# Optimization experiments

Measured on AMD Instinct MI355X. Metric: run time of the kernel, lower is better.

## Reference

```python
import jax, jax.numpy as jnp
import numpy as np

N = 65536   # query points
M = 65536   # support points
H = 32      # neighbors per query
IN = 64     # input feature dim
OUT = 64    # out_dim // 2
K = 15      # kernel points
EXTENT = 0.1 * 1.2 / 2.5  # radius * kp_extent / conv_radius = 0.048
BN_EPS = 1e-5


def setup_inputs() -> dict:
    key = jax.random.key(0)
    ks = jax.random.split(key, 8)
    x = jax.random.normal(ks[0], (M, IN), dtype=jnp.float32)
    q_pts = jax.random.uniform(ks[1], (N, 3), dtype=jnp.float32) * 0.1
    s_pts = jax.random.uniform(ks[2], (M, 3), dtype=jnp.float32) * 0.1
    neighb_inds = jax.random.randint(ks[3], (N, H), 0, M, dtype=jnp.int32)
    kernel_points = jax.random.normal(ks[4], (K, 3), dtype=jnp.float32) * (0.5 * EXTENT)
    weights = jax.random.normal(ks[5], (K, IN, OUT), dtype=jnp.float32) * 0.05
    gamma = jnp.ones((OUT,), dtype=jnp.float32)
    beta = jnp.zeros((OUT,), dtype=jnp.float32)
    return {"x": x, "q_pts": q_pts, "s_pts": s_pts, "neighb_inds": neighb_inds,
            "kernel_points": kernel_points, "weights": weights,
            "gamma": gamma, "beta": beta}


def reference(x, q_pts, s_pts, neighb_inds, kernel_points, weights, gamma, beta):
    # --- KPConv (rigid, linear influence, sum aggregation) ---
    # Shadow point/feature for out-of-range neighbor indices (KPConv convention).
    s_pad = jnp.concatenate([s_pts, jnp.full((1, 3), 1e6, s_pts.dtype)], axis=0)
    x_pad = jnp.concatenate([x, jnp.zeros((1, x.shape[1]), x.dtype)], axis=0)

    # Relative neighbor coordinates: [N, H, 3]
    neighbors = s_pad[neighb_inds] - q_pts[:, None, :]
    # Squared distance to each kernel point: [N, H, K]
    diffs = neighbors[:, :, None, :] - kernel_points[None, None, :, :]
    sq_dist = jnp.sum(diffs * diffs, axis=-1)
    # Linear kernel-point influence, clipped at 0: [N, H, K]
    all_weights = jnp.maximum(1.0 - jnp.sqrt(sq_dist) / EXTENT, 0.0)

    # Gather neighbor features: [N, H, IN]
    neighb_x = x_pad[neighb_inds]
    # Influence-weighted aggregation per kernel point: [N, K, IN]
    weighted = jnp.einsum('nhk,nhi->nki', all_weights, neighb_x)
    # Apply per-kernel-point weight matrices and sum over kernel points: [N, OUT]
    out = jnp.einsum('nki,kio->no', weighted, weights)

    # --- BatchNorm (training-mode statistics over points) ---
    mean = jnp.mean(out, axis=0)
    var = jnp.var(out, axis=0)
    out = (out - mean) / jnp.sqrt(var + BN_EPS) * gamma + beta

    # --- LeakyReLU(0.1) ---
    return jnp.where(out >= 0, out, 0.1 * out)
```

## Files before the change

kernel.cpp:

```cpp
#include <hip/hip_runtime.h>
#include <math.h>

#define NQ   65536
#define H    32
#define IN   64
#define OUTC 64
#define K    15
#define QB   16
#define INV_EXT (1.0f / 0.048f)

#define OFF_PSUM  131072
#define OFF_SCSH  (OFF_PSUM + 2097152)
#define OFF_XBF   (OFF_SCSH + 1024)
#define NEED_BF16 (OFF_XBF + (size_t)NQ * IN * 2)

typedef __attribute__((ext_vector_type(8))) short short8;
typedef __attribute__((ext_vector_type(4))) short short4v;
typedef __attribute__((ext_vector_type(4))) float float4v;

static __device__ __forceinline__ unsigned short f2bf(float f) {
    return (unsigned short)((__float_as_uint(f) + 0x8000u) >> 16);
}
static __device__ __forceinline__ unsigned pk2(float a, float b) {
    return (__float_as_uint(a) + 0x8000u) >> 16 |
           ((__float_as_uint(b) + 0x8000u) & 0xFFFF0000u);
}

__global__ __launch_bounds__(256) void prep_all(
    const float* __restrict__ W, const float* __restrict__ x,
    short* __restrict__ Bfrag, unsigned short* __restrict__ xbf, int do_x)
{
    const int b = blockIdx.x;
    if (b < 4096) {
        if (do_x) {
            const int t = b * 256 + threadIdx.x;
            const float4 v = ((const float4*)x)[t];
            uint2 p; p.x = pk2(v.x, v.y); p.y = pk2(v.z, v.w);
            ((uint2*)xbf)[t] = p;
        }
    } else {
        const int t2  = (b - 4096) * 256 + threadIdx.x;
        const int j   = t2 & 7;
        const int ln  = (t2 >> 3) & 63;
        const int tt  = (t2 >> 9) & 31;
        const int wvq = t2 >> 14;
        const int kp2 = tt * 32 + (ln >> 4) * 8 + j;
        const int kq  = kp2 & 15;
        const int ii  = kp2 >> 4;
        const int oo  = wvq * 16 + (ln & 15);
        const float val = (kq < K) ? W[(kq * 64 + ii) * 64 + oo] : 0.0f;
        Bfrag[t2] = (short)f2bf(val);
    }
}

template<bool BFX>
__global__ __launch_bounds__(256, 5) void kpconv_mfma(
    const float* __restrict__ x, const unsigned short* __restrict__ xbf,
    const float* __restrict__ qp, const float* __restrict__ sp,
    const int* __restrict__ inds, const float* __restrict__ kp,
    const short* __restrict__ Bfrag, float* __restrict__ out_raw,
    float* __restrict__ psum)
{
    __shared__ __align__(16) short lds[16384];
    short* xn  = lds;
    short* wT2 = lds + 8192;

    const int tid  = threadIdx.x;
    const int lane = tid & 63;
    const int wv   = tid >> 6;
    const int quad = lane >> 4;
    const int ml   = lane & 15;
    const int q0   = blockIdx.x * QB;

    const int q8x = (((lane >> 3) & 1) << 2) | (lane & 3);
    const int m8x = (((lane >> 4) & 3) << 1) | ((lane >> 2) & 1);
    const int hbase = ((q8x >> 2) << 4) | (q8x & 3);

    short* xn_own = xn + wv * 2048;

    short8 xv[4][4];
    float4 xf[4][4][2];
#pragma unroll
    for (int qi = 0; qi < 4; ++qi) {
        const int ibase = (q0 + wv * 4 + qi) * H;
#pragma unroll
        for (int j = 0; j < 4; ++j) {
            const int id = inds[ibase + hbase + j * 4];
            if (BFX) {
                xv[qi][j] = *(const short8*)((const short*)xbf + id * IN + m8x * 8);
            } else {
                xf[qi][j][0] = *(const float4*)(x + id * IN + m8x * 8);
                xf[qi][j][1] = *(const float4*)(x + id * IN + m8x * 8 + 4);
            }
        }
    }

#pragma unroll
    for (int rep = 0; rep < 2; ++rep) {
        const int p  = lane + rep * 64;
        const int qi = p >> 5, h = p & 31;
        const int qg = wv * 4 + qi;
        const int n  = q0 + qg;
        const int id = inds[n * H + h];
        const float dx = sp[id * 3 + 0] - qp[n * 3 + 0];
        const float dy = sp[id * 3 + 1] - qp[n * 3 + 1];
        const float dz = sp[id * 3 + 2] - qp[n * 3 + 2];
        short8 w0, w1;
#pragma unroll
        for (int k = 0; k < K; ++k) {
            const float ex = dx - kp[k * 3 + 0];
            const float ey = dy - kp[k * 3 + 1];
            const float ez = dz - kp[k * 3 + 2];
            const float sq = ex * ex + ey * ey + ez * ez;
            float wval = 1.0f - __builtin_amdgcn_sqrtf(sq) * INV_EXT;
            wval = wval > 0.0f ? wval : 0.0f;
            if (k < 8) w0[k]     = (short)f2bf(wval);
            else       w1[k - 8] = (short)f2bf(wval);
        }
        w1[7] = 0;
        short* dst = wT2 + qg * 512 + ((h >> 2) & 1) * 256 + (h >> 3) * 64 + (h & 3) * 16;
        *(short8*)dst       = w0;
        *(short8*)(dst + 8) = w1;
    }

    const unsigned ldsb = (unsigned)(size_t)(&lds[0]);
    const unsigned xnb  = ldsb + (unsigned)(wv * 4096 + lane * 8);
    const unsigned wtb  = ldsb + 16384u + (unsigned)(wv * 4096 + lane * 8);

    float4v frag[4][4];
#pragma unroll
    for (int qi = 0; qi < 4; ++qi)
#pragma unroll
        for (int v = 0; v < 4; ++v) frag[qi][v] = (float4v){0.f, 0.f, 0.f, 0.f};

    const int EbBase = (m8x >> 1) * 512 + (q8x >> 2) * 128 + (q8x & 3) * 16 + (m8x & 1) * 8;

#pragma unroll
    for (int qi = 0; qi < 4; ++qi) {
#pragma unroll
        for (int j = 0; j < 4; ++j) {
            short8 pv;
            if (BFX) {
                pv = xv[qi][j];
            } else {
                const float4 a0 = xf[qi][j][0], a1 = xf[qi][j][1];
                pv[0] = (short)f2bf(a0.x); pv[1] = (short)f2bf(a0.y);
                pv[2] = (short)f2bf(a0.z); pv[3] = (short)f2bf(a0.w);
                pv[4] = (short)f2bf(a1.x); pv[5] = (short)f2bf(a1.y);
                pv[6] = (short)f2bf(a1.z); pv[7] = (short)f2bf(a1.w);
            }
            *(short8*)&xn_own[EbBase + (j & 1) * 256 + (j >> 1) * 64] = pv;
        }
        __builtin_amdgcn_sched_barrier(0);

        short4v a0, a1, b0[4], b1[4];
        asm volatile("ds_read_b64_tr_b16 %0, %1 offset:%c2"
                     : "=v"(a0) : "v"(wtb), "i"(qi * 1024) : "memory");
        asm volatile("ds_read_b64_tr_b16 %0, %1 offset:%c2"
                     : "=v"(a1) : "v"(wtb), "i"(qi * 1024 + 512) : "memory");
#pragma unroll
        for (int v = 0; v < 4; ++v) {
            asm volatile("ds_read_b64_tr_b16 %0, %1 offset:%c2"
                         : "=v"(b0[v]) : "v"(xnb), "i"(v * 1024) : "memory");
            asm volatile("ds_read_b64_tr_b16 %0, %1 offset:%c2"
                         : "=v"(b1[v]) : "v"(xnb), "i"(v * 1024 + 512) : "memory");
        }
        asm volatile("s_waitcnt lgkmcnt(0)");
        __builtin_amdgcn_sched_barrier(0);

        short8 a;
#pragma unroll
        for (int e = 0; e < 4; ++e) { a[e] = a0[e]; a[e + 4] = a1[e]; }
#pragma unroll
        for (int v = 0; v < 4; ++v) {
            short8 bb;
#pragma unroll
            for (int e = 0; e < 4; ++e) { bb[e] = b0[v][e]; bb[e + 4] = b1[v][e]; }
            frag[qi][v] = __builtin_amdgcn_mfma_f32_16x16x32_bf16(a, bb, frag[qi][v], 0, 0, 0);
        }
    }

    __syncthreads();

    char* AwtB = (char*)lds;
#pragma unroll
    for (int qi = 0; qi < 4; ++qi) {
        const int qg = wv * 4 + qi;
        char* qb = AwtB + qg * 2048;
        const int xr = ((qg & 7) << 4) ^ (((qg >> 3) & 1) << 3) ^ ((ml >> 2) << 3);
#pragma unroll
        for (int v = 0; v < 4; ++v) {
            short4v w;
#pragma unroll
            for (int r = 0; r < 4; ++r) w[r] = (short)f2bf(frag[qi][v][r]);
            const int Bw = (v * 16 + ml) * 32 + quad * 8;
            *(short4v*)(qb + (Bw ^ xr)) = w;
        }
    }
    __syncthreads();

    float4v acc = (float4v){0.f, 0.f, 0.f, 0.f};
    const short* bptr = Bfrag + (wv * 32) * 512 + lane * 8;
    const char*  arow = AwtB + ml * 2048;
    const int    xr2  = ((ml & 7) << 4) ^ (((ml >> 3) & 1) << 3);
#pragma unroll 2
    for (int t = 0; t < 32; ++t) {
        const int Br = t * 64 + quad * 16;
        const int ad = (Br ^ xr2 ^ (((t >> 1) & 3) << 3));
        const short4v alo = *(const short4v*)(arow + ad);
        const short4v ahi = *(const short4v*)(arow + (ad ^ 8));
        short8 a;
#pragma unroll
        for (int e = 0; e < 4; ++e) { a[e] = alo[e]; a[e + 4] = ahi[e]; }
        const short8 bb = *(const short8*)(bptr + t * 512);
        acc = __builtin_amdgcn_mfma_f32_16x16x32_bf16(a, bb, acc, 0, 0, 0);
    }

    float s = 0.f, s2 = 0.f;
#pragma unroll
    for (int r = 0; r < 4; ++r) {
        const float v = acc[r];
        out_raw[(q0 + quad * 4 + r) * OUTC + wv * 16 + ml] = v;
        s += v; s2 += v * v;
    }
    s  += __shfl_xor(s, 16, 64);  s  += __shfl_xor(s, 32, 64);
    s2 += __shfl_xor(s2, 16, 64); s2 += __shfl_xor(s2, 32, 64);
    if (quad == 0) {
        const int c = wv * 16 + ml;
        psum[c * 4096 + blockIdx.x]          = s;
        psum[262144 + c * 4096 + blockIdx.x] = s2;
    }
}

__global__ __launch_bounds__(256) void bn_stats(
    const float* __restrict__ psum, const float* __restrict__ gamma,
    const float* __restrict__ beta, float* __restrict__ sc_sh)
{
    const int c = blockIdx.x;
    const int t = threadIdx.x;
    float s = 0.f, q = 0.f;
#pragma unroll
    for (int i = 0; i < 16; ++i) {
        s += psum[c * 4096 + t + i * 256];
        q += psum[262144 + c * 4096 + t + i * 256];
    }
    __shared__ float rs[4], rq[4];
#pragma unroll
    for (int off = 32; off; off >>= 1) {
        s += __shfl_down(s, off, 64);
        q += __shfl_down(q, off, 64);
    }
    if ((t & 63) == 0) { rs[t >> 6] = s; rq[t >> 6] = q; }
    __syncthreads();
    if (t == 0) {
        s = rs[0] + rs[1] + rs[2] + rs[3];
        q = rq[0] + rq[1] + rq[2] + rq[3];
        const float mean = s * (1.0f / (float)NQ);
        const float var  = q * (1.0f / (float)NQ) - mean * mean;
        const float scale = gamma[c] / sqrtf(var + 1e-5f);
        sc_sh[c]      = scale;
        sc_sh[64 + c] = beta[c] - mean * scale;
    }
}

__global__ __launch_bounds__(256) void bn_apply(
    float* __restrict__ out, const float* __restrict__ sc_sh)
{
    __shared__ float sc[64];
    __shared__ float sh[64];
    if (threadIdx.x < 64) {
        sc[threadIdx.x] = sc_sh[threadIdx.x];
        sh[threadIdx.x] = sc_sh[64 + threadIdx.x];
    }
    __syncthreads();
    const int idx = blockIdx.x * 256 + threadIdx.x;
#pragma unroll
    for (int it = 0; it < 4; ++it) {
        const int e = idx + it * 262144;
        float4 v = ((const float4*)out)[e];
        const int cg = (e & 15) * 4;
        float4 r;
        r.x = v.x * sc[cg + 0] + sh[cg + 0];
        r.y = v.y * sc[cg + 1] + sh[cg + 1];
        r.z = v.z * sc[cg + 2] + sh[cg + 2];
        r.w = v.w * sc[cg + 3] + sh[cg + 3];
        r.x = r.x >= 0.0f ? r.x : 0.1f * r.x;
        r.y = r.y >= 0.0f ? r.y : 0.1f * r.y;
        r.z = r.z >= 0.0f ? r.z : 0.1f * r.z;
        r.w = r.w >= 0.0f ? r.w : 0.1f * r.w;
        ((float4*)out)[e] = r;
    }
}

extern "C" void kernel_launch(void* const* d_in, const int* in_sizes, int n_in,
                              void* d_out, int out_size, void* d_ws, size_t ws_size,
                              hipStream_t stream)
{
    (void)in_sizes; (void)n_in; (void)out_size;
    const float* x     = (const float*)d_in[0];
    const float* qp    = (const float*)d_in[1];
    const float* sp    = (const float*)d_in[2];
    const int*   inds  = (const int*)d_in[3];
    const float* kp    = (const float*)d_in[4];
    const float* W     = (const float*)d_in[5];
    const float* gamma = (const float*)d_in[6];
    const float* beta  = (const float*)d_in[7];
    float* out = (float*)d_out;

    short*          Bfrag = (short*)d_ws;
    float*          psum  = (float*)((char*)d_ws + OFF_PSUM);
    float*          sc_sh = (float*)((char*)d_ws + OFF_SCSH);
    unsigned short* xbf   = (unsigned short*)((char*)d_ws + OFF_XBF);

    const int use_bf = (ws_size >= NEED_BF16) ? 1 : 0;

    prep_all<<<4352, 256, 0, stream>>>(W, x, Bfrag, xbf, use_bf);
    if (use_bf)
        kpconv_mfma<true><<<NQ / QB, 256, 0, stream>>>(x, xbf, qp, sp, inds, kp, Bfrag, out, psum);
    else
        kpconv_mfma<false><<<NQ / QB, 256, 0, stream>>>(x, xbf, qp, sp, inds, kp, Bfrag, out, psum);
    bn_stats<<<64, 256, 0, stream>>>(psum, gamma, beta, sc_sh);
    bn_apply<<<1024, 256, 0, stream>>>(out, sc_sh);
}
```

Measured before the change: 160.6 us.

## Pad LDS feature layout, simplify gather mapping, and split MFMA accumulator chain

```diff
diff --git a/kernel.cpp b/kernel.cpp
--- a/kernel.cpp
+++ b/kernel.cpp
@@ -63,34 +63,32 @@
 {
     __shared__ __align__(16) short lds[16384];
     short* xn  = lds;
-    short* wT2 = lds + 8192;
+    short* wT2 = lds + 8448;
 
     const int tid  = threadIdx.x;
     const int lane = tid & 63;
     const int wv   = tid >> 6;
     const int quad = lane >> 4;
     const int ml   = lane & 15;
+    const int q8   = lane >> 3;
+    const int m8   = lane & 7;
     const int q0   = blockIdx.x * QB;
 
-    const int q8x = (((lane >> 3) & 1) << 2) | (lane & 3);
-    const int m8x = (((lane >> 4) & 3) << 1) | ((lane >> 2) & 1);
-    const int hbase = ((q8x >> 2) << 4) | (q8x & 3);
-
-    short* xn_own = xn + wv * 2048;
-
-    short8 xv[4][4];
-    float4 xf[4][4][2];
+    short* xn_own = xn + wv * 2112;
+
+    short8  xv[4][4];
+    float4v xf[4][4][2];
 #pragma unroll
     for (int qi = 0; qi < 4; ++qi) {
         const int ibase = (q0 + wv * 4 + qi) * H;
 #pragma unroll
         for (int j = 0; j < 4; ++j) {
-            const int id = inds[ibase + hbase + j * 4];
+            const int id = inds[ibase + j * 8 + q8];
             if (BFX) {
-                xv[qi][j] = *(const short8*)((const short*)xbf + id * IN + m8x * 8);
+                xv[qi][j] = *(const short8*)((const short*)xbf + id * IN + m8 * 8);
             } else {
-                xf[qi][j][0] = *(const float4*)(x + id * IN + m8x * 8);
-                xf[qi][j][1] = *(const float4*)(x + id * IN + m8x * 8 + 4);
+                xf[qi][j][0] = *(const float4v*)(x + id * IN + m8 * 8);
+                xf[qi][j][1] = *(const float4v*)(x + id * IN + m8 * 8 + 4);
             }
         }
     }
@@ -123,9 +121,21 @@
         *(short8*)(dst + 8) = w1;
     }
 
+#pragma unroll
+    for (int qi = 0; qi < 3; ++qi)
+#pragma unroll
+        for (int j = 0; j < 4; ++j) {
+            if (BFX) {
+                asm volatile("" :: "v"(xv[qi][j]));
+            } else {
+                asm volatile("" :: "v"(xf[qi][j][0]));
+                asm volatile("" :: "v"(xf[qi][j][1]));
+            }
+        }
+
     const unsigned ldsb = (unsigned)(size_t)(&lds[0]);
-    const unsigned xnb  = ldsb + (unsigned)(wv * 4096 + lane * 8);
-    const unsigned wtb  = ldsb + 16384u + (unsigned)(wv * 4096 + lane * 8);
+    const unsigned xnb  = ldsb + (unsigned)(wv * 4224 + lane * 8);
+    const unsigned wtb  = ldsb + 16896u + (unsigned)(wv * 4096 + lane * 8);
 
     float4v frag[4][4];
 #pragma unroll
@@ -133,7 +143,7 @@
 #pragma unroll
         for (int v = 0; v < 4; ++v) frag[qi][v] = (float4v){0.f, 0.f, 0.f, 0.f};
 
-    const int EbBase = (m8x >> 1) * 512 + (q8x >> 2) * 128 + (q8x & 3) * 16 + (m8x & 1) * 8;
+    const int Eb = (m8 >> 1) * 528 + ((q8 >> 2) & 1) * 256 + (q8 & 3) * 16 + (m8 & 1) * 8;
 
 #pragma unroll
     for (int qi = 0; qi < 4; ++qi) {
@@ -143,13 +153,13 @@
             if (BFX) {
                 pv = xv[qi][j];
             } else {
-                const float4 a0 = xf[qi][j][0], a1 = xf[qi][j][1];
-                pv[0] = (short)f2bf(a0.x); pv[1] = (short)f2bf(a0.y);
-                pv[2] = (short)f2bf(a0.z); pv[3] = (short)f2bf(a0.w);
-                pv[4] = (short)f2bf(a1.x); pv[5] = (short)f2bf(a1.y);
-                pv[6] = (short)f2bf(a1.z); pv[7] = (short)f2bf(a1.w);
+                const float4v a0 = xf[qi][j][0], a1 = xf[qi][j][1];
+                pv[0] = (short)f2bf(a0[0]); pv[1] = (short)f2bf(a0[1]);
+                pv[2] = (short)f2bf(a0[2]); pv[3] = (short)f2bf(a0[3]);
+                pv[4] = (short)f2bf(a1[0]); pv[5] = (short)f2bf(a1[1]);
+                pv[6] = (short)f2bf(a1[2]); pv[7] = (short)f2bf(a1[3]);
             }
-            *(short8*)&xn_own[EbBase + (j & 1) * 256 + (j >> 1) * 64] = pv;
+            *(short8*)&xn_own[Eb + j * 64] = pv;
         }
         __builtin_amdgcn_sched_barrier(0);
 
@@ -161,9 +171,9 @@
 #pragma unroll
         for (int v = 0; v < 4; ++v) {
             asm volatile("ds_read_b64_tr_b16 %0, %1 offset:%c2"
-                         : "=v"(b0[v]) : "v"(xnb), "i"(v * 1024) : "memory");
+                         : "=v"(b0[v]) : "v"(xnb), "i"(v * 1056) : "memory");
             asm volatile("ds_read_b64_tr_b16 %0, %1 offset:%c2"
-                         : "=v"(b1[v]) : "v"(xnb), "i"(v * 1024 + 512) : "memory");
+                         : "=v"(b1[v]) : "v"(xnb), "i"(v * 1056 + 512) : "memory");
         }
         asm volatile("s_waitcnt lgkmcnt(0)");
         __builtin_amdgcn_sched_barrier(0);
@@ -199,22 +209,38 @@
     }
     __syncthreads();
 
-    float4v acc = (float4v){0.f, 0.f, 0.f, 0.f};
+    float4v acc0 = (float4v){0.f, 0.f, 0.f, 0.f};
+    float4v acc1 = (float4v){0.f, 0.f, 0.f, 0.f};
     const short* bptr = Bfrag + (wv * 32) * 512 + lane * 8;
     const char*  arow = AwtB + ml * 2048;
     const int    xr2  = ((ml & 7) << 4) ^ (((ml >> 3) & 1) << 3);
 #pragma unroll 2
-    for (int t = 0; t < 32; ++t) {
-        const int Br = t * 64 + quad * 16;
-        const int ad = (Br ^ xr2 ^ (((t >> 1) & 3) << 3));
-        const short4v alo = *(const short4v*)(arow + ad);
-        const short4v ahi = *(const short4v*)(arow + (ad ^ 8));
-        short8 a;
-#pragma unroll
-        for (int e = 0; e < 4; ++e) { a[e] = alo[e]; a[e + 4] = ahi[e]; }
-        const short8 bb = *(const short8*)(bptr + t * 512);
-        acc = __builtin_amdgcn_mfma_f32_16x16x32_bf16(a, bb, acc, 0, 0, 0);
-    }
+    for (int t = 0; t < 32; t += 2) {
+        {
+            const int Br = t * 64 + quad * 16;
+            const int ad = Br ^ xr2 ^ (((t >> 1) & 3) << 3);
+            const short4v alo = *(const short4v*)(arow + ad);
+            const short4v ahi = *(const short4v*)(arow + (ad ^ 8));
+            short8 a;
+#pragma unroll
+            for (int e = 0; e < 4; ++e) { a[e] = alo[e]; a[e + 4] = ahi[e]; }
+            const short8 bb = *(const short8*)(bptr + t * 512);
+            acc0 = __builtin_amdgcn_mfma_f32_16x16x32_bf16(a, bb, acc0, 0, 0, 0);
+        }
+        {
+            const int t1 = t + 1;
+            const int Br = t1 * 64 + quad * 16;
+            const int ad = Br ^ xr2 ^ (((t1 >> 1) & 3) << 3);
+            const short4v alo = *(const short4v*)(arow + ad);
+            const short4v ahi = *(const short4v*)(arow + (ad ^ 8));
+            short8 a;
+#pragma unroll
+            for (int e = 0; e < 4; ++e) { a[e] = alo[e]; a[e + 4] = ahi[e]; }
+            const short8 bb = *(const short8*)(bptr + t1 * 512);
+            acc1 = __builtin_amdgcn_mfma_f32_16x16x32_bf16(a, bb, acc1, 0, 0, 0);
+        }
+    }
+    const float4v acc = acc0 + acc1;
 
     float s = 0.f, s2 = 0.f;
 #pragma unroll
```

Result: faster. 145.5 us (-9.4%).
